# Kernel tuning notes

Hardware: AMD Instinct MI355X
Metric: run time of the kernel (lower is better)

Reference implementation:

```python
import jax, jax.numpy as jnp
import numpy as np

RADIUS = 8
EPS = 0.01


def _xdiff(h, r):
    # box-sum along H (axis 2) from cumsum via shifted-slice differences
    l = h[:, :, r:2 * r + 1]
    m = h[:, :, 2 * r + 1:] - h[:, :, :-2 * r - 1]
    rr = h[:, :, -1:] - h[:, :, -2 * r - 1:-r - 1]
    return jnp.concatenate([l, m, rr], axis=2)


def _ydiff(h, r):
    # box-sum along W (axis 3)
    l = h[:, :, :, r:2 * r + 1]
    m = h[:, :, :, 2 * r + 1:] - h[:, :, :, :-2 * r - 1]
    rr = h[:, :, :, -1:] - h[:, :, :, -2 * r - 1:-r - 1]
    return jnp.concatenate([l, m, rr], axis=3)


def mean_filter(x, r):
    return _ydiff(jnp.cumsum(_xdiff(jnp.cumsum(x, axis=2), r), axis=3), r)


def setup_inputs() -> dict:
    key = jax.random.key(0)
    k1, k2 = jax.random.split(key)
    shape = (8, 3, 1024, 1024)
    x = jax.random.uniform(k1, shape, dtype=jnp.float32)
    y = jax.random.uniform(k2, shape, dtype=jnp.float32)
    return {"x": x, "y": y}


def reference(x, y):
    r = RADIUS
    b, c, h, w = x.shape
    mask = jnp.ones((1, 1, h, w), dtype=x.dtype)
    nump = mean_filter(mask, r)  # per-pixel window counts (handles borders)
    x_mean = mean_filter(x, r) / nump
    y_mean = mean_filter(y, r) / nump
    xy_cov = mean_filter(x * y, r) / nump - x_mean * y_mean
    x_var = mean_filter(x * x, r) / nump - x_mean * x_mean
    a = xy_cov / (x_var + EPS)
    a_mean = mean_filter(a, r) / nump
    b_mean = mean_filter(y_mean - a * x_mean, r) / nump
    return a_mean * x + b_mean
```

## Files before the change

kernel.cpp:

```cpp
#include <hip/hip_runtime.h>


namespace {
constexpr int RAD  = 8;
constexpr int H    = 1024;
constexpr int W    = 1024;
constexpr int NSL  = 24;
constexpr int ROWS = 32;
constexpr int PW   = W + 2 * RAD;
constexpr float EPS_C = 0.01f;
constexpr int GRID = NSL * (H / ROWS);
}

__device__ __forceinline__ float frcp(float v) { return __builtin_amdgcn_rcpf(v); }
__device__ __forceinline__ float4 z4() { return make_float4(0.f, 0.f, 0.f, 0.f); }

struct V4 { float4 x, y, xy, xx; };

__device__ __forceinline__ void vzero(V4& S) { S.x = z4(); S.y = z4(); S.xy = z4(); S.xx = z4(); }

__device__ __forceinline__ void vadd(V4& S, const float4 xv, const float4 yv) {
  S.x.x += xv.x; S.x.y += xv.y; S.x.z += xv.z; S.x.w += xv.w;
  S.y.x += yv.x; S.y.y += yv.y; S.y.z += yv.z; S.y.w += yv.w;
  S.xy.x += xv.x * yv.x; S.xy.y += xv.y * yv.y; S.xy.z += xv.z * yv.z; S.xy.w += xv.w * yv.w;
  S.xx.x += xv.x * xv.x; S.xx.y += xv.y * xv.y; S.xx.z += xv.z * xv.z; S.xx.w += xv.w * xv.w;
}

__device__ __forceinline__ void vsub(V4& S, const float4 xv, const float4 yv) {
  S.x.x -= xv.x; S.x.y -= xv.y; S.x.z -= xv.z; S.x.w -= xv.w;
  S.y.x -= yv.x; S.y.y -= yv.y; S.y.z -= yv.z; S.y.w -= yv.w;
  S.xy.x -= xv.x * yv.x; S.xy.y -= xv.y * yv.y; S.xy.z -= xv.z * yv.z; S.xy.w -= xv.w * yv.w;
  S.xx.x -= xv.x * xv.x; S.xx.y -= xv.y * xv.y; S.xx.z -= xv.z * xv.z; S.xx.w -= xv.w * xv.w;
}

__device__ __forceinline__ void map_block(int g, int& slice, int& r0) {
  const int xcd = g & 7;
  const int i = g >> 3;
  const int band = xcd * 4 + (i & 3);
  slice = i >> 2;
  r0 = band * ROWS;
}

__device__ __forceinline__ void hbox(const float* buf, int c0, float o[4]) {
  const float4 va = *reinterpret_cast<const float4*>(buf + c0);
  const float4 vb = *reinterpret_cast<const float4*>(buf + c0 + 4);
  const float4 vc = *reinterpret_cast<const float4*>(buf + c0 + 8);
  const float4 vd = *reinterpret_cast<const float4*>(buf + c0 + 12);
  const float4 ve = *reinterpret_cast<const float4*>(buf + c0 + 16);
  const float w[20] = {va.x, va.y, va.z, va.w, vb.x, vb.y, vb.z, vb.w,
                       vc.x, vc.y, vc.z, vc.w, vd.x, vd.y, vd.z, vd.w,
                       ve.x, ve.y, ve.z, ve.w};
  float s = w[0];
#pragma unroll
  for (int k = 1; k <= 16; ++k) s += w[k];
  o[0] = s;
  o[1] = o[0] - w[0] + w[17];
  o[2] = o[1] - w[1] + w[18];
  o[3] = o[2] - w[2] + w[19];
}

__device__ __forceinline__ float inv_cnt(int p) {
  int lo = p - RAD < 0 ? 0 : p - RAD;
  int hi = p + RAD > H - 1 ? H - 1 : p + RAD;
  return frcp((float)(hi - lo + 1));
}

__device__ __forceinline__ float4 ldrow(const float* __restrict__ s, int r, int c0) {
  return *reinterpret_cast<const float4*>(s + (size_t)r * W + c0);
}

__device__ __forceinline__ void publish(float* fbase, int c0, const V4& S) {
  *reinterpret_cast<float4*>(&fbase[0 * PW + RAD + c0]) = S.x;
  *reinterpret_cast<float4*>(&fbase[1 * PW + RAD + c0]) = S.y;
  *reinterpret_cast<float4*>(&fbase[2 * PW + RAD + c0]) = S.xy;
  *reinterpret_cast<float4*>(&fbase[3 * PW + RAD + c0]) = S.xx;
}

__device__ __forceinline__ void compute_ab(const float* fbase, int c0, float invcy,
                                           const float invcx[4], float av[4], float bv[4]) {
  float bx[4], by[4], bxy[4], bxx[4];
  hbox(fbase + 0 * PW, c0, bx);
  hbox(fbase + 1 * PW, c0, by);
  hbox(fbase + 2 * PW, c0, bxy);
  hbox(fbase + 3 * PW, c0, bxx);
#pragma unroll
  for (int j = 0; j < 4; ++j) {
    const float invN = invcy * invcx[j];
    const float mx = bx[j] * invN;
    const float my = by[j] * invN;
    const float cov = bxy[j] * invN - mx * my;
    const float var = bxx[j] * invN - mx * mx;
    const float a = cov * frcp(var + EPS_C);
    av[j] = a;
    bv[j] = my - a * mx;
  }
}

__device__ __forceinline__ void publish2(float* sbase, int c0, const float av[4], const float bv[4]) {
  *reinterpret_cast<float4*>(&sbase[RAD + c0]) = make_float4(av[0], av[1], av[2], av[3]);
  *reinterpret_cast<float4*>(&sbase[PW + RAD + c0]) = make_float4(bv[0], bv[1], bv[2], bv[3]);
}

__device__ __forceinline__ void hbox2(const float* sbase, int c0, float HA[4], float HB[4]) {
  hbox(sbase, c0, HA);
  hbox(sbase + PW, c0, HB);
}

__global__ __launch_bounds__(256, 3) void k_fused(
    const float* __restrict__ x, const float* __restrict__ y, float* __restrict__ out) {
  __shared__ float stage[12 * PW];
  float* fL = stage;
  float* fG = stage + 4 * PW;
  float* sL = stage + 8 * PW;
  float* sG = stage + 10 * PW;

  const int t = threadIdx.x;
  int slice, r0;
  map_block(blockIdx.x, slice, r0);
  const size_t soff = (size_t)slice * H * W;
  const float* xs = x + soff;
  const float* ys = y + soff;
  float* os = out + soff;
  const int c0 = t << 2;

  if (t < 96) {
    const int j = t >> 3, tt = t & 7;
    stage[j * PW + tt] = 0.f;
    stage[j * PW + W + RAD + tt] = 0.f;
  }

  float invcx[4];
#pragma unroll
  for (int j = 0; j < 4; ++j) {
    const int c = c0 + j;
    const int cl = c - RAD < 0 ? 0 : c - RAD;
    const int ch = c + RAD > W - 1 ? W - 1 : c + RAD;
    invcx[j] = frcp((float)(ch - cl + 1));
  }

  const int cstart = (r0 - 9 < 0) ? 0 : (r0 - 9);
  V4 SL; vzero(SL);
  {
    int lo = cstart - RAD; if (lo < 0) lo = 0;
    for (int rr = lo; rr <= cstart + RAD; ++rr) {
      vadd(SL, ldrow(xs, rr, c0), ldrow(ys, rr, c0));
    }
  }
  V4 SG;
  if (r0 == 0) vzero(SG); else SG = SL;
  float4 Sa = z4(), Sb = z4();

  __syncthreads();

  for (int c = cstart; c <= r0 + 7; ++c) {
    const float4 xa = ldrow(xs, c + 9, c0), ya = ldrow(ys, c + 9, c0);
    float4 xr = z4(), yr = z4();
    if (c - RAD >= 0) { xr = ldrow(xs, c - RAD, c0); yr = ldrow(ys, c - RAD, c0); }

    publish(fL, c0, SL);
    __syncthreads();
    float av[4], bv[4];
    compute_ab(fL, c0, inv_cnt(c), invcx, av, bv);
    publish2(sL, c0, av, bv);
    __syncthreads();
    float HA[4], HB[4];
    hbox2(sL, c0, HA, HB);
    Sa.x += HA[0]; Sa.y += HA[1]; Sa.z += HA[2]; Sa.w += HA[3];
    Sb.x += HB[0]; Sb.y += HB[1]; Sb.z += HB[2]; Sb.w += HB[3];
    vadd(SL, xa, ya);
    vsub(SL, xr, yr);
    __syncthreads();
  }

  for (int k = r0; k < r0 + ROWS; ++k) {
    const float4 xk = ldrow(xs, k, c0), yk = ldrow(ys, k, c0);
    float4 xt = z4(), yt = z4(), xb = z4(), yb = z4();
    if (k + 17 < H)  { xt = ldrow(xs, k + 17, c0); yt = ldrow(ys, k + 17, c0); }
    if (k - 17 >= 0) { xb = ldrow(xs, k - 17, c0); yb = ldrow(ys, k - 17, c0); }

    publish(fL, c0, SL);
    publish(fG, c0, SG);
    __syncthreads();

    const int p = k + 8, q = k - 9;
    float avL[4], bvL[4], avG[4], bvG[4];
    compute_ab(fL, c0, inv_cnt(p), invcx, avL, bvL);
    compute_ab(fG, c0, inv_cnt(q), invcx, avG, bvG);
    publish2(sL, c0, avL, bvL);
    publish2(sG, c0, avG, bvG);
    __syncthreads();

    float HAL[4], HBL[4], HAG[4], HBG[4];
    hbox2(sL, c0, HAL, HBL);
    hbox2(sG, c0, HAG, HBG);
    if (p <= H - 1) {
      Sa.x += HAL[0]; Sa.y += HAL[1]; Sa.z += HAL[2]; Sa.w += HAL[3];
      Sb.x += HBL[0]; Sb.y += HBL[1]; Sb.z += HBL[2]; Sb.w += HBL[3];
    }
    if (q >= 0) {
      Sa.x -= HAG[0]; Sa.y -= HAG[1]; Sa.z -= HAG[2]; Sa.w -= HAG[3];
      Sb.x -= HBG[0]; Sb.y -= HBG[1]; Sb.z -= HBG[2]; Sb.w -= HBG[3];
    }

    const float invcy = inv_cnt(k);
    const float n0 = invcy * invcx[0], n1 = invcy * invcx[1];
    const float n2 = invcy * invcx[2], n3 = invcy * invcx[3];
    float4 o;
    o.x = Sa.x * n0 * xk.x + Sb.x * n0;
    o.y = Sa.y * n1 * xk.y + Sb.y * n1;
    o.z = Sa.z * n2 * xk.z + Sb.z * n2;
    o.w = Sa.w * n3 * xk.w + Sb.w * n3;
    *reinterpret_cast<float4*>(os + (size_t)k * W + c0) = o;

    vadd(SL, xt, yt);
    vsub(SL, xk, yk);
    vadd(SG, xk, yk);
    vsub(SG, xb, yb);
    __syncthreads();
  }
}

extern "C" void kernel_launch(void* const* d_in, const int* in_sizes, int n_in,
                              void* d_out, int out_size, void* d_ws, size_t ws_size,
                              hipStream_t stream) {
  const float* x = (const float*)d_in[0];
  const float* y = (const float*)d_in[1];
  float* out = (float*)d_out;
  k_fused<<<GRID, 256, 0, stream>>>(x, y, out);
}
```

Before: 338.3 us.

## Rewrite guided filter with column tiles, fp16 a/b ring history, and single-window sums

The kernel is restructured into 512-column tiles of 64 rows with 128 threads, and halo columns are handled by a few extra threads. The second running vertical window is replaced by a 17-row ring buffer in shared memory that stores per-row a/b values packed as fp16, so the leaving row is subtracted from history instead of being recomputed. Each thread keeps its own centre values in registers rather than reloading them from LDS, and barriers become a raw waitcnt plus s_barrier. This removes duplicate hbox and abmath work and the extra row loads, but it adds halo redundancy, divergent edge threads, and fp16 rounding error that builds up in the running a/b sums.

```diff
diff --git a/kernel.cpp b/kernel.cpp
--- a/kernel.cpp
+++ b/kernel.cpp
@@ -1,222 +1,335 @@
 #include <hip/hip_runtime.h>
+#include <hip/hip_fp16.h>
 
 
 namespace {
-constexpr int RAD  = 8;
-constexpr int H    = 1024;
-constexpr int W    = 1024;
-constexpr int NSL  = 24;
-constexpr int ROWS = 32;
-constexpr int PW   = W + 2 * RAD;
+constexpr int RAD = 8;
+constexpr int H = 1024, W = 1024;
+constexpr int NSL = 24;
+constexpr int TW = 512;
+constexpr int ROWS = 64;
+constexpr int NT = 128;
+constexpr int VWID = TW + 32;
+constexpr int ABWID = TW + 16;
+constexpr int ABUN = ABWID / 4;
+constexpr int HD = 17;
 constexpr float EPS_C = 0.01f;
-constexpr int GRID = NSL * (H / ROWS);
+constexpr int GRID = NSL * (H / ROWS) * (W / TW);
 }
 
 __device__ __forceinline__ float frcp(float v) { return __builtin_amdgcn_rcpf(v); }
 __device__ __forceinline__ float4 z4() { return make_float4(0.f, 0.f, 0.f, 0.f); }
 
-struct V4 { float4 x, y, xy, xx; };
-
-__device__ __forceinline__ void vzero(V4& S) { S.x = z4(); S.y = z4(); S.xy = z4(); S.xx = z4(); }
-
-__device__ __forceinline__ void vadd(V4& S, const float4 xv, const float4 yv) {
-  S.x.x += xv.x; S.x.y += xv.y; S.x.z += xv.z; S.x.w += xv.w;
-  S.y.x += yv.x; S.y.y += yv.y; S.y.z += yv.z; S.y.w += yv.w;
-  S.xy.x += xv.x * yv.x; S.xy.y += xv.y * yv.y; S.xy.z += xv.z * yv.z; S.xy.w += xv.w * yv.w;
-  S.xx.x += xv.x * xv.x; S.xx.y += xv.y * xv.y; S.xx.z += xv.z * xv.z; S.xx.w += xv.w * xv.w;
-}
-
-__device__ __forceinline__ void vsub(V4& S, const float4 xv, const float4 yv) {
-  S.x.x -= xv.x; S.x.y -= xv.y; S.x.z -= xv.z; S.x.w -= xv.w;
-  S.y.x -= yv.x; S.y.y -= yv.y; S.y.z -= yv.z; S.y.w -= yv.w;
-  S.xy.x -= xv.x * yv.x; S.xy.y -= xv.y * yv.y; S.xy.z -= xv.z * yv.z; S.xy.w -= xv.w * yv.w;
-  S.xx.x -= xv.x * xv.x; S.xx.y -= xv.y * xv.y; S.xx.z -= xv.z * xv.z; S.xx.w -= xv.w * xv.w;
-}
-
-__device__ __forceinline__ void map_block(int g, int& slice, int& r0) {
-  const int xcd = g & 7;
-  const int i = g >> 3;
-  const int band = xcd * 4 + (i & 3);
-  slice = i >> 2;
-  r0 = band * ROWS;
-}
-
-__device__ __forceinline__ void hbox(const float* buf, int c0, float o[4]) {
-  const float4 va = *reinterpret_cast<const float4*>(buf + c0);
-  const float4 vb = *reinterpret_cast<const float4*>(buf + c0 + 4);
-  const float4 vc = *reinterpret_cast<const float4*>(buf + c0 + 8);
-  const float4 vd = *reinterpret_cast<const float4*>(buf + c0 + 12);
-  const float4 ve = *reinterpret_cast<const float4*>(buf + c0 + 16);
+__device__ __forceinline__ void bar_lgkm() {
+  asm volatile("s_waitcnt lgkmcnt(0)\n\ts_barrier" ::: "memory");
+}
+
+__device__ __forceinline__ float inv_span(int p, int n) {
+  int lo = p - RAD; lo = lo < 0 ? 0 : lo;
+  int hi = p + RAD; hi = hi > n - 1 ? n - 1 : hi;
+  return frcp((float)(hi - lo + 1));
+}
+
+__device__ __forceinline__ float4 ld4(const float* __restrict__ b, int r, int c) {
+  return *reinterpret_cast<const float4*>(b + (size_t)r * W + c);
+}
+
+struct VQ { float4 x, y, xy, xx; };
+__device__ __forceinline__ void vq_zero(VQ& S) { S.x = z4(); S.y = z4(); S.xy = z4(); S.xx = z4(); }
+__device__ __forceinline__ void vq_add(VQ& S, const float4 a, const float4 b) {
+  S.x.x += a.x; S.x.y += a.y; S.x.z += a.z; S.x.w += a.w;
+  S.y.x += b.x; S.y.y += b.y; S.y.z += b.z; S.y.w += b.w;
+  S.xy.x += a.x * b.x; S.xy.y += a.y * b.y; S.xy.z += a.z * b.z; S.xy.w += a.w * b.w;
+  S.xx.x += a.x * a.x; S.xx.y += a.y * a.y; S.xx.z += a.z * a.z; S.xx.w += a.w * a.w;
+}
+__device__ __forceinline__ void vq_sub(VQ& S, const float4 a, const float4 b) {
+  S.x.x -= a.x; S.x.y -= a.y; S.x.z -= a.z; S.x.w -= a.w;
+  S.y.x -= b.x; S.y.y -= b.y; S.y.z -= b.z; S.y.w -= b.w;
+  S.xy.x -= a.x * b.x; S.xy.y -= a.y * b.y; S.xy.z -= a.z * b.z; S.xy.w -= a.w * b.w;
+  S.xx.x -= a.x * a.x; S.xx.y -= a.y * a.y; S.xx.z -= a.z * a.z; S.xx.w -= a.w * a.w;
+}
+
+__device__ __forceinline__ void hcomb(const float* w, float o[4]) {
+  float s = w[0];
+#pragma unroll
+  for (int i = 1; i <= 16; ++i) s += w[i];
+  o[0] = s;
+  o[1] = s - w[0] + w[17];
+  o[2] = o[1] - w[1] + w[18];
+  o[3] = o[2] - w[2] + w[19];
+}
+
+__device__ __forceinline__ void hbox_own(const float* buf, int base, float4 mid, float o[4]) {
+  const float4 va = *reinterpret_cast<const float4*>(buf + base);
+  const float4 vb = *reinterpret_cast<const float4*>(buf + base + 4);
+  const float4 vd = *reinterpret_cast<const float4*>(buf + base + 12);
+  const float4 ve = *reinterpret_cast<const float4*>(buf + base + 16);
+  const float w[20] = {va.x, va.y, va.z, va.w, vb.x, vb.y, vb.z, vb.w,
+                       mid.x, mid.y, mid.z, mid.w, vd.x, vd.y, vd.z, vd.w,
+                       ve.x, ve.y, ve.z, ve.w};
+  hcomb(w, o);
+}
+
+__device__ __forceinline__ void hbox_full(const float* buf, int base, float o[4]) {
+  const float4 va = *reinterpret_cast<const float4*>(buf + base);
+  const float4 vb = *reinterpret_cast<const float4*>(buf + base + 4);
+  const float4 vc = *reinterpret_cast<const float4*>(buf + base + 8);
+  const float4 vd = *reinterpret_cast<const float4*>(buf + base + 12);
+  const float4 ve = *reinterpret_cast<const float4*>(buf + base + 16);
   const float w[20] = {va.x, va.y, va.z, va.w, vb.x, vb.y, vb.z, vb.w,
                        vc.x, vc.y, vc.z, vc.w, vd.x, vd.y, vd.z, vd.w,
                        ve.x, ve.y, ve.z, ve.w};
-  float s = w[0];
-#pragma unroll
-  for (int k = 1; k <= 16; ++k) s += w[k];
-  o[0] = s;
-  o[1] = o[0] - w[0] + w[17];
-  o[2] = o[1] - w[1] + w[18];
-  o[3] = o[2] - w[2] + w[19];
-}
-
-__device__ __forceinline__ float inv_cnt(int p) {
-  int lo = p - RAD < 0 ? 0 : p - RAD;
-  int hi = p + RAD > H - 1 ? H - 1 : p + RAD;
-  return frcp((float)(hi - lo + 1));
-}
-
-__device__ __forceinline__ float4 ldrow(const float* __restrict__ s, int r, int c0) {
-  return *reinterpret_cast<const float4*>(s + (size_t)r * W + c0);
-}
-
-__device__ __forceinline__ void publish(float* fbase, int c0, const V4& S) {
-  *reinterpret_cast<float4*>(&fbase[0 * PW + RAD + c0]) = S.x;
-  *reinterpret_cast<float4*>(&fbase[1 * PW + RAD + c0]) = S.y;
-  *reinterpret_cast<float4*>(&fbase[2 * PW + RAD + c0]) = S.xy;
-  *reinterpret_cast<float4*>(&fbase[3 * PW + RAD + c0]) = S.xx;
-}
-
-__device__ __forceinline__ void compute_ab(const float* fbase, int c0, float invcy,
-                                           const float invcx[4], float av[4], float bv[4]) {
-  float bx[4], by[4], bxy[4], bxx[4];
-  hbox(fbase + 0 * PW, c0, bx);
-  hbox(fbase + 1 * PW, c0, by);
-  hbox(fbase + 2 * PW, c0, bxy);
-  hbox(fbase + 3 * PW, c0, bxx);
+  hcomb(w, o);
+}
+
+__device__ __forceinline__ void abmath(const float bx[4], const float by[4],
+                                       const float bxy[4], const float bxx[4],
+                                       float icy, const float icx[4],
+                                       float a[4], float b[4]) {
 #pragma unroll
   for (int j = 0; j < 4; ++j) {
-    const float invN = invcy * invcx[j];
-    const float mx = bx[j] * invN;
-    const float my = by[j] * invN;
-    const float cov = bxy[j] * invN - mx * my;
-    const float var = bxx[j] * invN - mx * mx;
-    const float a = cov * frcp(var + EPS_C);
-    av[j] = a;
-    bv[j] = my - a * mx;
-  }
-}
-
-__device__ __forceinline__ void publish2(float* sbase, int c0, const float av[4], const float bv[4]) {
-  *reinterpret_cast<float4*>(&sbase[RAD + c0]) = make_float4(av[0], av[1], av[2], av[3]);
-  *reinterpret_cast<float4*>(&sbase[PW + RAD + c0]) = make_float4(bv[0], bv[1], bv[2], bv[3]);
-}
-
-__device__ __forceinline__ void hbox2(const float* sbase, int c0, float HA[4], float HB[4]) {
-  hbox(sbase, c0, HA);
-  hbox(sbase + PW, c0, HB);
-}
-
-__global__ __launch_bounds__(256, 3) void k_fused(
-    const float* __restrict__ x, const float* __restrict__ y, float* __restrict__ out) {
-  __shared__ float stage[12 * PW];
-  float* fL = stage;
-  float* fG = stage + 4 * PW;
-  float* sL = stage + 8 * PW;
-  float* sG = stage + 10 * PW;
+    const float n = icy * icx[j];
+    const float mx = bx[j] * n, my = by[j] * n;
+    const float cov = bxy[j] * n - mx * my;
+    const float var = bxx[j] * n - mx * mx;
+    const float av = cov * frcp(var + EPS_C);
+    a[j] = av; b[j] = my - av * mx;
+  }
+}
+
+__device__ __forceinline__ uint4 packab(const float a[4], const float b[4]) {
+  union { uint4 u; __half2 h[4]; } P;
+  P.h[0] = __floats2half2_rn(a[0], a[1]);
+  P.h[1] = __floats2half2_rn(a[2], a[3]);
+  P.h[2] = __floats2half2_rn(b[0], b[1]);
+  P.h[3] = __floats2half2_rn(b[2], b[3]);
+  return P.u;
+}
+__device__ __forceinline__ void unpackab(uint4 u, float a[4], float b[4]) {
+  union { uint4 u; __half2 h[4]; } P; P.u = u;
+  const float2 f0 = __half22float2(P.h[0]);
+  const float2 f1 = __half22float2(P.h[1]);
+  const float2 f2 = __half22float2(P.h[2]);
+  const float2 f3 = __half22float2(P.h[3]);
+  a[0] = f0.x; a[1] = f0.y; a[2] = f1.x; a[3] = f1.y;
+  b[0] = f2.x; b[1] = f2.y; b[2] = f3.x; b[3] = f3.y;
+}
+
+__device__ __forceinline__ void acc4(float4& d, const float s[4]) {
+  d.x += s[0]; d.y += s[1]; d.z += s[2]; d.w += s[3];
+}
+__device__ __forceinline__ void dec4(float4& d, const float s[4]) {
+  d.x -= s[0]; d.y -= s[1]; d.z -= s[2]; d.w -= s[3];
+}
+
+__global__ __launch_bounds__(NT, 2) void k_gf(const float* __restrict__ x,
+                                              const float* __restrict__ y,
+                                              float* __restrict__ out) {
+  __shared__ float fS[4][VWID];
+  __shared__ float sAB[2][ABWID];
+  __shared__ uint4 hist[HD][ABUN];
 
   const int t = threadIdx.x;
-  int slice, r0;
-  map_block(blockIdx.x, slice, r0);
-  const size_t soff = (size_t)slice * H * W;
-  const float* xs = x + soff;
-  const float* ys = y + soff;
-  float* os = out + soff;
-  const int c0 = t << 2;
-
-  if (t < 96) {
-    const int j = t >> 3, tt = t & 7;
-    stage[j * PW + tt] = 0.f;
-    stage[j * PW + W + RAD + tt] = 0.f;
-  }
-
-  float invcx[4];
+  int g = blockIdx.x;
+  const int xcd = g & 7; g >>= 3;
+  const int band = xcd * 2 + (g & 1); g >>= 1;
+  const int ctile = g & 1; g >>= 1;
+  const int slice = g;
+  const int r0 = band * ROWS;
+  const int C0 = ctile * TW;
+
+  const float* xs = x + (size_t)slice * H * W;
+  const float* ys = y + (size_t)slice * H * W;
+  float* os = out + (size_t)slice * H * W;
+
+  const int vMc = C0 - 8 + 4 * t;
+  const bool vMact = vMc >= 0;
+  const int uE = (t < 2) ? t : (128 + t);
+  const int vEc = C0 - 16 + 4 * uE;
+  const bool vEact = (t < 8) && (vEc >= 0) && (vEc < W);
+  const bool abMact = vMact;
+  const int wE = 128 + (t - 64);
+  const int aEc = C0 - 8 + 4 * wE;
+  const bool abEact = (t >= 64) && (t < 68) && (aEc < W);
+  const int sIdx = (t >= 2) ? (t - 2) : (126 + t);
+  const int oc = C0 + 4 * sIdx;
+  const bool outMain = (t >= 2);
+
+  float icxA[4], icxO[4], icxE[4];
 #pragma unroll
   for (int j = 0; j < 4; ++j) {
-    const int c = c0 + j;
-    const int cl = c - RAD < 0 ? 0 : c - RAD;
-    const int ch = c + RAD > W - 1 ? W - 1 : c + RAD;
-    invcx[j] = frcp((float)(ch - cl + 1));
-  }
+    icxA[j] = inv_span(vMc + j, W);
+    icxO[j] = inv_span(oc + j, W);
+    icxE[j] = inv_span(aEc + j, W);
+  }
+
+  for (int i = t; i < 4 * VWID; i += NT) (&fS[0][0])[i] = 0.f;
+  for (int i = t; i < 2 * ABWID; i += NT) (&sAB[0][0])[i] = 0.f;
+  __syncthreads();
+
+  VQ M, E; vq_zero(M); vq_zero(E);
+  float4 VaM = z4(), VbM = z4(), VaE = z4(), VbE = z4();
 
   const int cstart = (r0 - 9 < 0) ? 0 : (r0 - 9);
-  V4 SL; vzero(SL);
   {
     int lo = cstart - RAD; if (lo < 0) lo = 0;
     for (int rr = lo; rr <= cstart + RAD; ++rr) {
-      vadd(SL, ldrow(xs, rr, c0), ldrow(ys, rr, c0));
-    }
-  }
-  V4 SG;
-  if (r0 == 0) vzero(SG); else SG = SL;
-  float4 Sa = z4(), Sb = z4();
-
-  __syncthreads();
+      if (vMact) vq_add(M, ld4(xs, rr, vMc), ld4(ys, rr, vMc));
+      if (vEact) vq_add(E, ld4(xs, rr, vEc), ld4(ys, rr, vEc));
+    }
+  }
 
   for (int c = cstart; c <= r0 + 7; ++c) {
-    const float4 xa = ldrow(xs, c + 9, c0), ya = ldrow(ys, c + 9, c0);
-    float4 xr = z4(), yr = z4();
-    if (c - RAD >= 0) { xr = ldrow(xs, c - RAD, c0); yr = ldrow(ys, c - RAD, c0); }
-
-    publish(fL, c0, SL);
-    __syncthreads();
-    float av[4], bv[4];
-    compute_ab(fL, c0, inv_cnt(c), invcx, av, bv);
-    publish2(sL, c0, av, bv);
-    __syncthreads();
-    float HA[4], HB[4];
-    hbox2(sL, c0, HA, HB);
-    Sa.x += HA[0]; Sa.y += HA[1]; Sa.z += HA[2]; Sa.w += HA[3];
-    Sb.x += HB[0]; Sb.y += HB[1]; Sb.z += HB[2]; Sb.w += HB[3];
-    vadd(SL, xa, ya);
-    vsub(SL, xr, yr);
-    __syncthreads();
+    const int ra = c + 9, rs = c - RAD;
+    float4 xa = z4(), ya = z4(), xr = z4(), yr = z4();
+    float4 xae = z4(), yae = z4(), xre = z4(), yre = z4();
+    if (vMact) {
+      xa = ld4(xs, ra, vMc); ya = ld4(ys, ra, vMc);
+      if (rs >= 0) { xr = ld4(xs, rs, vMc); yr = ld4(ys, rs, vMc); }
+    }
+    if (vEact) {
+      xae = ld4(xs, ra, vEc); yae = ld4(ys, ra, vEc);
+      if (rs >= 0) { xre = ld4(xs, rs, vEc); yre = ld4(ys, rs, vEc); }
+    }
+    if (vMact) {
+      *reinterpret_cast<float4*>(&fS[0][4 * (t + 2)]) = M.x;
+      *reinterpret_cast<float4*>(&fS[1][4 * (t + 2)]) = M.y;
+      *reinterpret_cast<float4*>(&fS[2][4 * (t + 2)]) = M.xy;
+      *reinterpret_cast<float4*>(&fS[3][4 * (t + 2)]) = M.xx;
+    }
+    if (vEact) {
+      *reinterpret_cast<float4*>(&fS[0][4 * uE]) = E.x;
+      *reinterpret_cast<float4*>(&fS[1][4 * uE]) = E.y;
+      *reinterpret_cast<float4*>(&fS[2][4 * uE]) = E.xy;
+      *reinterpret_cast<float4*>(&fS[3][4 * uE]) = E.xx;
+    }
+    bar_lgkm();
+    const float icy = inv_span(c, H);
+    if (abMact) {
+      float bx[4], by[4], bxy[4], bxx[4], a4[4], b4[4];
+      hbox_own(&fS[0][0], 4 * t, M.x, bx);
+      hbox_own(&fS[1][0], 4 * t, M.y, by);
+      hbox_own(&fS[2][0], 4 * t, M.xy, bxy);
+      hbox_own(&fS[3][0], 4 * t, M.xx, bxx);
+      abmath(bx, by, bxy, bxx, icy, icxA, a4, b4);
+      hist[c % HD][t] = packab(a4, b4);
+      acc4(VaM, a4); acc4(VbM, b4);
+    }
+    if (abEact) {
+      float bx[4], by[4], bxy[4], bxx[4], a4[4], b4[4];
+      hbox_full(&fS[0][0], 4 * wE, bx);
+      hbox_full(&fS[1][0], 4 * wE, by);
+      hbox_full(&fS[2][0], 4 * wE, bxy);
+      hbox_full(&fS[3][0], 4 * wE, bxx);
+      abmath(bx, by, bxy, bxx, icy, icxE, a4, b4);
+      hist[c % HD][wE] = packab(a4, b4);
+      acc4(VaE, a4); acc4(VbE, b4);
+    }
+    if (vMact) { vq_add(M, xa, ya); vq_sub(M, xr, yr); }
+    if (vEact) { vq_add(E, xae, yae); vq_sub(E, xre, yre); }
+    bar_lgkm();
   }
 
   for (int k = r0; k < r0 + ROWS; ++k) {
-    const float4 xk = ldrow(xs, k, c0), yk = ldrow(ys, k, c0);
-    float4 xt = z4(), yt = z4(), xb = z4(), yb = z4();
-    if (k + 17 < H)  { xt = ldrow(xs, k + 17, c0); yt = ldrow(ys, k + 17, c0); }
-    if (k - 17 >= 0) { xb = ldrow(xs, k - 17, c0); yb = ldrow(ys, k - 17, c0); }
-
-    publish(fL, c0, SL);
-    publish(fG, c0, SG);
-    __syncthreads();
+    const int ra = k + 17;
+    const bool doA = ra < H;
+    float4 xa = z4(), ya = z4(), xk = z4(), yk = z4();
+    float4 xae = z4(), yae = z4(), xke = z4(), yke = z4(), xo2 = z4();
+    if (vMact) {
+      if (doA) { xa = ld4(xs, ra, vMc); ya = ld4(ys, ra, vMc); }
+      xk = ld4(xs, k, vMc); yk = ld4(ys, k, vMc);
+    }
+    if (vEact) {
+      if (doA) { xae = ld4(xs, ra, vEc); yae = ld4(ys, ra, vEc); }
+      xke = ld4(xs, k, vEc); yke = ld4(ys, k, vEc);
+    }
+    if (t < 2) xo2 = ld4(xs, k, oc);
+    if (vMact) {
+      *reinterpret_cast<float4*>(&fS[0][4 * (t + 2)]) = M.x;
+      *reinterpret_cast<float4*>(&fS[1][4 * (t + 2)]) = M.y;
+      *reinterpret_cast<float4*>(&fS[2][4 * (t + 2)]) = M.xy;
+      *reinterpret_cast<float4*>(&fS[3][4 * (t + 2)]) = M.xx;
+    }
+    if (vEact) {
+      *reinterpret_cast<float4*>(&fS[0][4 * uE]) = E.x;
+      *reinterpret_cast<float4*>(&fS[1][4 * uE]) = E.y;
+      *reinterpret_cast<float4*>(&fS[2][4 * uE]) = E.xy;
+      *reinterpret_cast<float4*>(&fS[3][4 * uE]) = E.xx;
+    }
+    bar_lgkm();
 
     const int p = k + 8, q = k - 9;
-    float avL[4], bvL[4], avG[4], bvG[4];
-    compute_ab(fL, c0, inv_cnt(p), invcx, avL, bvL);
-    compute_ab(fG, c0, inv_cnt(q), invcx, avG, bvG);
-    publish2(sL, c0, avL, bvL);
-    publish2(sG, c0, avG, bvG);
-    __syncthreads();
-
-    float HAL[4], HBL[4], HAG[4], HBG[4];
-    hbox2(sL, c0, HAL, HBL);
-    hbox2(sG, c0, HAG, HBG);
-    if (p <= H - 1) {
-      Sa.x += HAL[0]; Sa.y += HAL[1]; Sa.z += HAL[2]; Sa.w += HAL[3];
-      Sb.x += HBL[0]; Sb.y += HBL[1]; Sb.z += HBL[2]; Sb.w += HBL[3];
-    }
-    if (q >= 0) {
-      Sa.x -= HAG[0]; Sa.y -= HAG[1]; Sa.z -= HAG[2]; Sa.w -= HAG[3];
-      Sb.x -= HBG[0]; Sb.y -= HBG[1]; Sb.z -= HBG[2]; Sb.w -= HBG[3];
-    }
-
-    const float invcy = inv_cnt(k);
-    const float n0 = invcy * invcx[0], n1 = invcy * invcx[1];
-    const float n2 = invcy * invcx[2], n3 = invcy * invcx[3];
+    const float icyp = inv_span(p, H);
+    if (abMact) {
+      float a4[4] = {0, 0, 0, 0}, b4[4] = {0, 0, 0, 0};
+      if (p < H) {
+        float bx[4], by[4], bxy[4], bxx[4];
+        hbox_own(&fS[0][0], 4 * t, M.x, bx);
+        hbox_own(&fS[1][0], 4 * t, M.y, by);
+        hbox_own(&fS[2][0], 4 * t, M.xy, bxy);
+        hbox_own(&fS[3][0], 4 * t, M.xx, bxx);
+        abmath(bx, by, bxy, bxx, icyp, icxA, a4, b4);
+      }
+      if (q >= 0) {
+        float aq[4], bq[4];
+        unpackab(hist[q % HD][t], aq, bq);
+        dec4(VaM, aq); dec4(VbM, bq);
+      }
+      if (p < H) {
+        hist[p % HD][t] = packab(a4, b4);
+        acc4(VaM, a4); acc4(VbM, b4);
+      }
+      *reinterpret_cast<float4*>(&sAB[0][4 * t]) = VaM;
+      *reinterpret_cast<float4*>(&sAB[1][4 * t]) = VbM;
+    }
+    if (abEact) {
+      float a4[4] = {0, 0, 0, 0}, b4[4] = {0, 0, 0, 0};
+      if (p < H) {
+        float bx[4], by[4], bxy[4], bxx[4];
+        hbox_full(&fS[0][0], 4 * wE, bx);
+        hbox_full(&fS[1][0], 4 * wE, by);
+        hbox_full(&fS[2][0], 4 * wE, bxy);
+        hbox_full(&fS[3][0], 4 * wE, bxx);
+        abmath(bx, by, bxy, bxx, icyp, icxE, a4, b4);
+      }
+      if (q >= 0) {
+        float aq[4], bq[4];
+        unpackab(hist[q % HD][wE], aq, bq);
+        dec4(VaE, aq); dec4(VbE, bq);
+      }
+      if (p < H) {
+        hist[p % HD][wE] = packab(a4, b4);
+        acc4(VaE, a4); acc4(VbE, b4);
+      }
+      *reinterpret_cast<float4*>(&sAB[0][4 * wE]) = VaE;
+      *reinterpret_cast<float4*>(&sAB[1][4 * wE]) = VbE;
+    }
+    bar_lgkm();
+
+    float Sa[4], Sb[4];
+    if (outMain) {
+      hbox_own(&sAB[0][0], 4 * sIdx, VaM, Sa);
+      hbox_own(&sAB[1][0], 4 * sIdx, VbM, Sb);
+    } else {
+      hbox_full(&sAB[0][0], 4 * sIdx, Sa);
+      hbox_full(&sAB[1][0], 4 * sIdx, Sb);
+    }
+    const float icy = inv_span(k, H);
+    const float4 xv = outMain ? xk : xo2;
     float4 o;
-    o.x = Sa.x * n0 * xk.x + Sb.x * n0;
-    o.y = Sa.y * n1 * xk.y + Sb.y * n1;
-    o.z = Sa.z * n2 * xk.z + Sb.z * n2;
-    o.w = Sa.w * n3 * xk.w + Sb.w * n3;
-    *reinterpret_cast<float4*>(os + (size_t)k * W + c0) = o;
-
-    vadd(SL, xt, yt);
-    vsub(SL, xk, yk);
-    vadd(SG, xk, yk);
-    vsub(SG, xb, yb);
-    __syncthreads();
+    {
+      const float n0 = icy * icxO[0], n1 = icy * icxO[1];
+      const float n2 = icy * icxO[2], n3 = icy * icxO[3];
+      o.x = Sa[0] * n0 * xv.x + Sb[0] * n0;
+      o.y = Sa[1] * n1 * xv.y + Sb[1] * n1;
+      o.z = Sa[2] * n2 * xv.z + Sb[2] * n2;
+      o.w = Sa[3] * n3 * xv.w + Sb[3] * n3;
+    }
+    *reinterpret_cast<float4*>(os + (size_t)k * W + oc) = o;
+
+    if (vMact) { vq_add(M, xa, ya); vq_sub(M, xk, yk); }
+    if (vEact) { vq_add(E, xae, yae); vq_sub(E, xke, yke); }
+    bar_lgkm();
   }
 }
 
@@ -226,5 +339,5 @@
   const float* x = (const float*)d_in[0];
   const float* y = (const float*)d_in[1];
   float* out = (float*)d_out;
-  k_fused<<<GRID, 256, 0, stream>>>(x, y, out);
-}
+  k_gf<<<GRID, NT, 0, stream>>>(x, y, out);
+}
```

New measurement: 367.1 us. 1.09x slower.
